# Kernel tuning notes

Measured on AMD Instinct MI355X. Metric: run time of the kernel, lower is better.

The kernel has to match this reference:

```python
import jax, jax.numpy as jnp
import numpy as np

WS = 16  # window_size

def _conv1x1(x, w, b):
    # x: [n,c,h,w], w: [out,in], b: [out]
    return jnp.einsum('nchw,oc->nohw', x, w) + b[None, :, None, None]

def _se_attention(x, w1, b1, w2, b2):
    # global avg pool -> conv -> relu -> conv -> sigmoid; returns [n,C,1,1]
    p = x.mean(axis=(2, 3), keepdims=True)
    h = jax.nn.relu(_conv1x1(p, w1, b1))
    return jax.nn.sigmoid(_conv1x1(h, w2, b2))

def setup_inputs() -> dict:
    key = jax.random.key(0)
    ks = jax.random.split(key, 13)
    B, C, H, W = 8, 96, 256, 256
    Cr = C // 3
    s = 0.02
    return {
        'x': jax.random.normal(ks[0], (B, C, H, W), jnp.float32),
        'w_real': jax.random.normal(ks[1], (C, C), jnp.float32) * s,
        'b_real': jnp.zeros((C,), jnp.float32),
        'w_imag': jax.random.normal(ks[2], (C, C), jnp.float32) * s,
        'b_imag': jnp.zeros((C,), jnp.float32),
        'car_w1': jax.random.normal(ks[3], (Cr, C), jnp.float32) * s,
        'car_b1': jnp.zeros((Cr,), jnp.float32),
        'car_w2': jax.random.normal(ks[4], (C, Cr), jnp.float32) * s,
        'car_b2': jnp.zeros((C,), jnp.float32),
        'cai_w1': jax.random.normal(ks[5], (Cr, C), jnp.float32) * s,
        'cai_b1': jnp.zeros((Cr,), jnp.float32),
        'cai_w2': jax.random.normal(ks[6], (C, Cr), jnp.float32) * s,
        'cai_b2': jnp.zeros((C,), jnp.float32),
    }

def reference(x, w_real, b_real, w_imag, b_imag,
              car_w1, car_b1, car_w2, car_b2,
              cai_w1, cai_b1, cai_w2, cai_b2):
    B, C, H, W = x.shape
    nH, nW = H // WS, W // WS
    # window partition: [B,C,H,W] -> [B*nH*nW, C, WS, WS]
    xw = x.reshape(B, C, nH, WS, nW, WS)
    xw = xw.transpose(0, 2, 4, 1, 3, 5).reshape(-1, C, WS, WS)
    # 2D FFT per window, ortho norm
    x_fft = jnp.fft.fft2(xw, norm='ortho')
    real_conv = _conv1x1(jnp.real(x_fft), w_real, b_real)
    imag_conv = _conv1x1(jnp.imag(x_fft), w_imag, b_imag)
    real_att = _se_attention(real_conv, car_w1, car_b1, car_w2, car_b2)
    imag_att = _se_attention(imag_conv, cai_w1, cai_b1, cai_w2, cai_b2)
    real_conv = real_conv * (1.0 + real_att)
    imag_conv = imag_conv * (1.0 + imag_att)
    x_fft_enh = jax.lax.complex(real_conv, imag_conv)
    x_ifft = jnp.real(jnp.fft.ifft2(x_fft_enh, norm='ortho'))
    # window merge: [B*nH*nW, C, WS, WS] -> [B,C,H,W]
    out = x_ifft.reshape(B, nH, nW, C, WS, WS)
    out = out.transpose(0, 3, 1, 4, 2, 5).reshape(B, C, H, W)
    return out
```

## Files before the change

### kernel.cpp

```cpp
#include <hip/hip_runtime.h>
#include <hip/hip_bf16.h>
#include <math.h>

#define NWIN 2048

typedef __bf16 v8bf __attribute__((ext_vector_type(8)));
typedef __bf16 v2bf __attribute__((ext_vector_type(2)));
typedef float  v4f  __attribute__((ext_vector_type(4)));

__global__ __launch_bounds__(128) void se_alpha_kernel(
    const float* __restrict__ x,
    const float* __restrict__ w_real, const float* __restrict__ b_real,
    const float* __restrict__ car_w1, const float* __restrict__ car_b1,
    const float* __restrict__ car_w2, const float* __restrict__ car_b2,
    const float* __restrict__ b_imag,
    const float* __restrict__ cai_w1, const float* __restrict__ cai_b1,
    const float* __restrict__ cai_w2, const float* __restrict__ cai_b2,
    float* __restrict__ alpha, float* __restrict__ beta)
{
    __shared__ float wr_s[96 * 97];
    __shared__ float w1_s[32 * 97];
    __shared__ float w2_s[96 * 33];
    __shared__ float x0_s[96 * 17];
    __shared__ float pr_s[16 * 97];
    __shared__ float h1_s[16 * 33];
    const int t = threadIdx.x;
    const int blkid = blockIdx.x;

    if (blkid < 128) {
        const int b = blkid >> 4, wh = blkid & 15;
        for (int idx = t; idx < 96 * 96; idx += 128) {
            int o = idx / 96, c = idx - o * 96;
            wr_s[o * 97 + c] = w_real[idx];
        }
        for (int idx = t; idx < 32 * 96; idx += 128) {
            int j = idx / 96, c = idx - j * 96;
            w1_s[j * 97 + c] = car_w1[idx];
        }
        for (int idx = t; idx < 96 * 32; idx += 128) {
            int o = idx >> 5, j = idx & 31;
            w2_s[o * 33 + j] = car_w2[idx];
        }
        for (int idx = t; idx < 96 * 16; idx += 128) {
            int c = idx >> 4, w = idx & 15;
            x0_s[c * 17 + w] = x[(((size_t)(b * 96 + c)) * 256 + wh * 16) * 256 + w * 16];
        }
        __syncthreads();
        #pragma unroll
        for (int i = 0; i < 12; ++i) {
            int p = t + i * 128;
            int o = p >> 4, w = p & 15;
            float acc = 0.f;
            #pragma unroll 4
            for (int c = 0; c < 96; ++c) acc += wr_s[o * 97 + c] * x0_s[c * 17 + w];
            pr_s[w * 97 + o] = acc * (1.0f / 16.0f) + b_real[o];
        }
        __syncthreads();
        #pragma unroll
        for (int i = 0; i < 4; ++i) {
            int p = t + i * 128;
            int j = p >> 4, w = p & 15;
            float acc = car_b1[j];
            #pragma unroll 4
            for (int o = 0; o < 96; ++o) acc += w1_s[j * 97 + o] * pr_s[w * 97 + o];
            h1_s[w * 33 + j] = fmaxf(acc, 0.f);
        }
        __syncthreads();
        #pragma unroll
        for (int i = 0; i < 12; ++i) {
            int p = t + i * 128;
            int o = p >> 4, w = p & 15;
            float acc = car_b2[o];
            #pragma unroll
            for (int j = 0; j < 32; ++j) acc += w2_s[o * 33 + j] * h1_s[w * 33 + j];
            int n = (blkid << 4) | w;
            alpha[(size_t)n * 96 + o] = 1.f + 1.f / (1.f + __expf(-acc));
        }
    } else {
        if (t < 32) {
            float acc = cai_b1[t];
            for (int o = 0; o < 96; ++o) acc += cai_w1[t * 96 + o] * b_imag[o];
            h1_s[t] = fmaxf(acc, 0.f);
        }
        __syncthreads();
        if (t < 96) {
            float acc = cai_b2[t];
            for (int j = 0; j < 32; ++j) acc += cai_w2[t * 32 + j] * h1_s[j];
            beta[t] = 1.f + 1.f / (1.f + __expf(-acc));
        }
    }
}

__global__ __launch_bounds__(1024, 4) void wfca_main_kernel(
    const float* __restrict__ x,
    const float* __restrict__ w_real, const float* __restrict__ w_imag,
    const float* __restrict__ b_real,
    const float* __restrict__ alpha, const float* __restrict__ beta,
    float* __restrict__ out)
{
    __shared__ __bf16 wr_s[96 * 104];
    __shared__ __bf16 wi_s[96 * 104];
    __shared__ float  xf[3][32 * 256];
    __shared__ float  alpha_s[768];

    const int t    = threadIdx.x;
    const int blk  = blockIdx.x;
    const int b    = blk >> 5;
    const int wh   = (blk >> 1) & 15;
    const int ww0  = (blk & 1) * 8;

    const int lane = t & 63;
    const int l16  = lane & 15;
    const int quad = lane >> 4;
    const int wv   = t >> 6;
    const int hf   = (16 - wv) & 15;
    const int wf   = (16 - l16) & 15;

    auto issue = [&](int w_, int k_) {
        #pragma unroll
        for (int u = 0; u < 2; ++u) {
            const int cl  = 2 * wv + u;
            const int swz = (cl >> 3) & 3;
            const float* g = x
                + (((size_t)(b * 96 + k_ * 32 + cl)) << 16)
                + (size_t)(wh * 16 + ((lane >> 2) ^ swz)) * 256
                + (ww0 + w_) * 16 + 4 * (lane & 3);
            float* l = &xf[k_][cl * 256];
            __builtin_amdgcn_global_load_lds(
                (const __attribute__((address_space(1))) float*)g,
                (__attribute__((address_space(3))) float*)l, 16, 0, 0);
        }
    };

    {
        float wrv[9], wiv[9], btv[9];
        #pragma unroll
        for (int r = 0; r < 9; ++r) {
            int idx = t + r * 1024;
            wrv[r] = w_real[idx];
            wiv[r] = w_imag[idx];
            btv[r] = beta[idx / 96];
        }
        #pragma unroll
        for (int r = 0; r < 9; ++r) {
            int idx = t + r * 1024;
            int o = idx / 96, c = idx - o * 96;
            wr_s[o * 104 + c] = (__bf16)(0.5f * wrv[r]);
            wi_s[o * 104 + c] = (__bf16)(0.5f * btv[r] * wiv[r]);
        }
    }
    if (t < 768) alpha_s[t] = alpha[(size_t)blk * 768 + t];
    float brv[6];
    #pragma unroll
    for (int n = 0; n < 6; ++n) brv[n] = b_real[n * 16 + l16];
    __syncthreads();

    issue(0, 0);
    issue(0, 1);

    const int pxq = (wv * 16 + l16) ^ (quad << 4);
    const int pfq = (hf * 16 + wf) ^ (quad << 4);

    for (int win = 0; win < 8; ++win) {
        float af[6];
        v4f acc[6];
        #pragma unroll
        for (int n = 0; n < 6; ++n) {
            af[n]  = alpha_s[win * 96 + n * 16 + l16];
            acc[n] = v4f{0.f, 0.f, 0.f, 0.f};
        }
        #pragma unroll
        for (int k = 0; k < 3; ++k) {
            if (win == 7 && k == 2)      asm volatile("s_waitcnt vmcnt(0)" ::: "memory");
            else if (win == 0 || k == 2) asm volatile("s_waitcnt vmcnt(2)" ::: "memory");
            else                         asm volatile("s_waitcnt vmcnt(8)" ::: "memory");
            __builtin_amdgcn_s_barrier();
            __builtin_amdgcn_sched_barrier(0);

            if (k == 0)      issue(win, 2);
            else if (k == 1) { if (win < 7) issue(win + 1, 0); }
            else             { if (win < 7) issue(win + 1, 1); }

            const float* xk = xf[k];
            float fx[8], ff[8];
            #pragma unroll
            for (int j = 0; j < 8; ++j) {
                fx[j] = xk[(quad * 8 + j) * 256 + pxq];
                ff[j] = xk[(quad * 8 + j) * 256 + pfq];
            }
            v8bf a_x, a_f, a_fn;
            #pragma unroll
            for (int j = 0; j < 8; ++j) {
                a_x[j]  = (__bf16)fx[j];
                a_f[j]  = (__bf16)ff[j];
                a_fn[j] = (__bf16)(-ff[j]);
            }
            const int c0 = k * 32;
            #pragma unroll
            for (int n = 0; n < 6; ++n) {
                v8bf bwr = *(const v8bf*)&wr_s[(n * 16 + l16) * 104 + c0 + quad * 8];
                v8bf bwi = *(const v8bf*)&wi_s[(n * 16 + l16) * 104 + c0 + quad * 8];
                acc[n] = __builtin_amdgcn_mfma_f32_16x16x32_bf16(a_x,  bwi, acc[n], 0, 0, 0);
                acc[n] = __builtin_amdgcn_mfma_f32_16x16x32_bf16(a_fn, bwi, acc[n], 0, 0, 0);
                v4f utmp = __builtin_amdgcn_mfma_f32_16x16x32_bf16(
                               a_x, bwr, v4f{0.f, 0.f, 0.f, 0.f}, 0, 0, 0);
                utmp = __builtin_amdgcn_mfma_f32_16x16x32_bf16(a_f, bwr, utmp, 0, 0, 0);
                #pragma unroll
                for (int r = 0; r < 4; ++r) acc[n][r] += af[n] * utmp[r];
            }
        }

        {
            const int col = (ww0 + win) * 16;
            #pragma unroll
            for (int n = 0; n < 6; ++n) {
                const int o = n * 16 + l16;
                v4f v = acc[n];
                if (wv == 0 && quad == 0) {
                    v[0] += 16.f * af[n] * brv[n];
                }
                size_t idx = (((size_t)(b * 96 + o)) * 256 + wh * 16 + wv) * 256
                             + col + quad * 4;
                *(v4f*)(out + idx) = v;
            }
        }
    }
}

extern "C" void kernel_launch(void* const* d_in, const int* in_sizes, int n_in,
                              void* d_out, int out_size, void* d_ws, size_t ws_size,
                              hipStream_t stream) {
    const float* x      = (const float*)d_in[0];
    const float* w_real = (const float*)d_in[1];
    const float* b_real = (const float*)d_in[2];
    const float* w_imag = (const float*)d_in[3];
    const float* b_imag = (const float*)d_in[4];
    const float* car_w1 = (const float*)d_in[5];
    const float* car_b1 = (const float*)d_in[6];
    const float* car_w2 = (const float*)d_in[7];
    const float* car_b2 = (const float*)d_in[8];
    const float* cai_w1 = (const float*)d_in[9];
    const float* cai_b1 = (const float*)d_in[10];
    const float* cai_w2 = (const float*)d_in[11];
    const float* cai_b2 = (const float*)d_in[12];
    float* out = (float*)d_out;

    float* alpha = (float*)d_ws;
    float* beta  = alpha + NWIN * 96;

    se_alpha_kernel<<<129, 128, 0, stream>>>(
        x, w_real, b_real, car_w1, car_b1, car_w2, car_b2,
        b_imag, cai_w1, cai_b1, cai_w2, cai_b2, alpha, beta);

    wfca_main_kernel<<<256, 1024, 0, stream>>>(
        x, w_real, w_imag, b_real, alpha, beta, out);
}
```

Before: 466.9 us.

## Process paired row pairs across eight windows instead of one window per iteration

The main loop now walks row pairs (h and its flipped partner 16-h) across eight adjacent windows at a time rather than one whole 16x16 window per iteration. Each global_load_lds now fetches two contiguous 512-byte row segments covering eight windows, which makes the reads wider and more coalesced, and the output stores for a row are likewise contiguous. Warps are remapped so each handles one window and either the low or high row, and the LDS swizzle and alpha indexing are adjusted to match. The risks are more complex index arithmetic and possible new LDS bank conflicts.

Result: faster. 419.2 us (-10.2%).

```diff
diff --git a/kernel.cpp b/kernel.cpp
--- a/kernel.cpp
+++ b/kernel.cpp
@@ -5,7 +5,6 @@
 #define NWIN 2048
 
 typedef __bf16 v8bf __attribute__((ext_vector_type(8)));
-typedef __bf16 v2bf __attribute__((ext_vector_type(2)));
 typedef float  v4f  __attribute__((ext_vector_type(4)));
 
 __global__ __launch_bounds__(128) void se_alpha_kernel(
@@ -107,25 +106,30 @@
     const int blk  = blockIdx.x;
     const int b    = blk >> 5;
     const int wh   = (blk >> 1) & 15;
-    const int ww0  = (blk & 1) * 8;
+    const int ch   = blk & 1;
 
     const int lane = t & 63;
     const int l16  = lane & 15;
     const int quad = lane >> 4;
     const int wv   = t >> 6;
-    const int hf   = (16 - wv) & 15;
-    const int wf   = (16 - l16) & 15;
-
-    auto issue = [&](int w_, int k_) {
+    const int r2m  = wv >> 3;
+    const int wm   = wv & 7;
+
+    const int pxq = (wm * 16 + l16) ^ ((quad & 1) << 4);
+    const int pfq = (wm * 16 + ((16 - l16) & 15)) ^ ((quad & 1) << 4);
+
+    auto issue = [&](int rp_, int k_, int buf_) {
+        const int hl = rp_;
+        const int hh = (rp_ == 0) ? 8 : 16 - rp_;
         #pragma unroll
         for (int u = 0; u < 2; ++u) {
-            const int cl  = 2 * wv + u;
-            const int swz = (cl >> 3) & 3;
-            const float* g = x
-                + (((size_t)(b * 96 + k_ * 32 + cl)) << 16)
-                + (size_t)(wh * 16 + ((lane >> 2) ^ swz)) * 256
-                + (ww0 + w_) * 16 + 4 * (lane & 3);
-            float* l = &xf[k_][cl * 256];
+            const int c    = 2 * wv + u;
+            const int swz  = ((c >> 3) & 1) << 4;
+            const int row  = (lane >> 5) ? hh : hl;
+            const int colg = (4 * (lane & 31)) ^ swz;
+            const float* g = x + (((size_t)(b * 96 + k_ * 32 + c)) << 16)
+                           + (size_t)(wh * 16 + row) * 256 + ch * 128 + colg;
+            float* l = &xf[buf_][c * 256];
             __builtin_amdgcn_global_load_lds(
                 (const __attribute__((address_space(1))) float*)g,
                 (__attribute__((address_space(3))) float*)l, 16, 0, 0);
@@ -149,51 +153,56 @@
             wi_s[o * 104 + c] = (__bf16)(0.5f * btv[r] * wiv[r]);
         }
     }
-    if (t < 768) alpha_s[t] = alpha[(size_t)blk * 768 + t];
+    if (t < 768) {
+        int w = t / 96, o = t - w * 96;
+        alpha_s[t] = alpha[(size_t)(b * 256 + wh * 16 + ch * 8 + w) * 96 + o];
+    }
     float brv[6];
     #pragma unroll
     for (int n = 0; n < 6; ++n) brv[n] = b_real[n * 16 + l16];
     __syncthreads();
 
-    issue(0, 0);
-    issue(0, 1);
-
-    const int pxq = (wv * 16 + l16) ^ (quad << 4);
-    const int pfq = (hf * 16 + wf) ^ (quad << 4);
-
-    for (int win = 0; win < 8; ++win) {
+    issue(0, 0, 0);
+    issue(0, 1, 1);
+
+    for (int rp = 0; rp < 8; ++rp) {
+        const int h_lo   = rp;
+        const int h_hi   = (rp == 0) ? 8 : 16 - rp;
+        const int h_out  = r2m ? h_hi : h_lo;
+        const int flipr2 = (rp == 0) ? r2m : 1 - r2m;
+
         float af[6];
         v4f acc[6];
         #pragma unroll
         for (int n = 0; n < 6; ++n) {
-            af[n]  = alpha_s[win * 96 + n * 16 + l16];
+            af[n]  = alpha_s[wm * 96 + n * 16 + l16];
             acc[n] = v4f{0.f, 0.f, 0.f, 0.f};
         }
         #pragma unroll
         for (int k = 0; k < 3; ++k) {
-            if (win == 7 && k == 2)      asm volatile("s_waitcnt vmcnt(0)" ::: "memory");
-            else if (win == 0 || k == 2) asm volatile("s_waitcnt vmcnt(2)" ::: "memory");
-            else                         asm volatile("s_waitcnt vmcnt(8)" ::: "memory");
+            if (rp == 7 && k == 2)      asm volatile("s_waitcnt vmcnt(0)" ::: "memory");
+            else if (rp == 0 || k == 2) asm volatile("s_waitcnt vmcnt(2)" ::: "memory");
+            else                        asm volatile("s_waitcnt vmcnt(8)" ::: "memory");
             __builtin_amdgcn_s_barrier();
             __builtin_amdgcn_sched_barrier(0);
 
-            if (k == 0)      issue(win, 2);
-            else if (k == 1) { if (win < 7) issue(win + 1, 0); }
-            else             { if (win < 7) issue(win + 1, 1); }
+            if (k == 0)      issue(rp, 2, 2);
+            else if (k == 1) { if (rp < 7) issue(rp + 1, 0, 0); }
+            else             { if (rp < 7) issue(rp + 1, 1, 1); }
 
             const float* xk = xf[k];
-            float fx[8], ff[8];
+            float fxv[8], ffv[8];
             #pragma unroll
             for (int j = 0; j < 8; ++j) {
-                fx[j] = xk[(quad * 8 + j) * 256 + pxq];
-                ff[j] = xk[(quad * 8 + j) * 256 + pfq];
+                fxv[j] = xk[(quad * 8 + j) * 256 + r2m * 128 + pxq];
+                ffv[j] = xk[(quad * 8 + j) * 256 + flipr2 * 128 + pfq];
             }
             v8bf a_x, a_f, a_fn;
             #pragma unroll
             for (int j = 0; j < 8; ++j) {
-                a_x[j]  = (__bf16)fx[j];
-                a_f[j]  = (__bf16)ff[j];
-                a_fn[j] = (__bf16)(-ff[j]);
+                a_x[j]  = (__bf16)fxv[j];
+                a_f[j]  = (__bf16)ffv[j];
+                a_fn[j] = (__bf16)(-ffv[j]);
             }
             const int c0 = k * 32;
             #pragma unroll
@@ -211,16 +220,15 @@
         }
 
         {
-            const int col = (ww0 + win) * 16;
             #pragma unroll
             for (int n = 0; n < 6; ++n) {
                 const int o = n * 16 + l16;
                 v4f v = acc[n];
-                if (wv == 0 && quad == 0) {
+                if (h_out == 0 && quad == 0) {
                     v[0] += 16.f * af[n] * brv[n];
                 }
-                size_t idx = (((size_t)(b * 96 + o)) * 256 + wh * 16 + wv) * 256
-                             + col + quad * 4;
+                size_t idx = (((size_t)(b * 96 + o)) * 256 + wh * 16 + h_out) * 256
+                             + ch * 128 + wm * 16 + quad * 4;
                 *(v4f*)(out + idx) = v;
             }
         }
```
